# Kernel tuning notes

Hardware: AMD Instinct MI355X
Metric: run time of the kernel (lower is better)

The kernel has to match this reference:

```python
import jax, jax.numpy as jnp
import numpy as np

GRID_SIZE = 0.04   # matches init_kwargs grid_size
AXIS_CAP = 32      # max voxel bins per axis (1/0.04 = 25 < 32); keeps keys in int32 range


def setup_inputs() -> dict:
    key = jax.random.key(0)
    k1, k2 = jax.random.split(key)
    N, C = 1_000_000, 64
    coord = jax.random.uniform(k1, (N, 3), dtype=jnp.float32)   # points in unit cube
    feat = jax.random.normal(k2, (N, C), dtype=jnp.float32)
    # cumulative per-batch point counts (pointops offset convention), 4 equal batches
    offset = jnp.array([N // 4, N // 2, 3 * N // 4, N], dtype=jnp.int32)
    return {"coord": coord, "feat": feat, "offset": offset}


def reference(coord, feat, offset):
    N = coord.shape[0]
    B = offset.shape[0]
    # batch id per point from cumulative offsets
    batch = jnp.searchsorted(offset, jnp.arange(N, dtype=offset.dtype), side='right')  # [N]
    batch = batch.astype(jnp.int32)
    # voxelize_helper: start = per-batch min coord (start=None path)
    start = jax.ops.segment_min(coord, batch, num_segments=B)            # [B,3]
    vox = jnp.floor((coord - start[batch]) / GRID_SIZE).astype(jnp.int32)  # [N,3]
    # fused (batch, voxel) key; batches never share keys
    vkey = ((batch * AXIS_CAP + vox[:, 0]) * AXIS_CAP + vox[:, 1]) * AXIS_CAP + vox[:, 2]
    # sorted cluster indices + CSR-style segment ids
    order = jnp.argsort(vkey)                                            # sorted_cluster_indices
    skey = vkey[order]
    new_seg = jnp.concatenate([jnp.zeros((1,), jnp.int32),
                               (skey[1:] != skey[:-1]).astype(jnp.int32)])
    seg = jnp.cumsum(new_seg)                                            # [N] segment id per sorted point
    n_vox = seg[-1] + 1                                                  # actual number of voxels (traced)
    # segment_csr(coord[order], reduce='mean')
    counts = jax.ops.segment_sum(jnp.ones((N,), coord.dtype), seg, num_segments=N)  # [N] padded
    coord_out = jax.ops.segment_sum(coord[order], seg, num_segments=N) / jnp.maximum(counts, 1.0)[:, None]
    # segment_csr(feat[order], reduce='max')
    feat_out = jax.ops.segment_max(feat[order], seg, num_segments=N)
    valid = jnp.arange(N) < n_vox                                        # [N] pad mask
    coord_out = jnp.where(valid[:, None], coord_out, 0.0)
    feat_out = jnp.where(valid[:, None], feat_out, 0.0)
    # batch[idx_ptr[:-1]] -> batch of first point in each segment, then batch2offset
    batch_out = jax.ops.segment_min(batch[order], seg, num_segments=N)
    batch_out = jnp.where(valid, batch_out, B)                           # padded rows -> bucket B
    per_batch = jax.ops.segment_sum(jnp.ones((N,), jnp.int32), batch_out, num_segments=B + 1)[:B]
    offset_out = jnp.cumsum(per_batch)                                   # [B]
    # outputs padded to N rows; first n_vox rows are the real voxels
    return coord_out, feat_out, offset_out, n_vox
```

## Files before the change

### kernel.cpp

```cpp
#include <hip/hip_runtime.h>
#include <hip/hip_bf16.h>
#include <cstdint>

#define AXIS_CAP 32
#define GRID_SIZE_F 0.04f
#define BINS_PER_BATCH (AXIS_CAP * AXIS_CAP * AXIS_CAP)
#define SCAN_TPB 256
#define BINS_PER_THREAD 4
#define BINS_PER_BLOCK (SCAN_TPB * BINS_PER_THREAD)
#define KC_PPT 4

typedef float f32x4 __attribute__((ext_vector_type(4)));
typedef uint32_t u32x2 __attribute__((ext_vector_type(2)));

__device__ __forceinline__ int point_batch(int i, const int* offs, int B) {
    int b = 0;
    for (int k = 0; k < B; ++k) b += (offs[k] <= i);
    return b;
}

__global__ void init_kernel(uint32_t* binCount, int nbins, int* startBits, int B) {
    int i = blockIdx.x * blockDim.x + threadIdx.x;
    int stride = gridDim.x * blockDim.x;
    for (int v = i; v < nbins; v += stride) binCount[v] = 0;
    if (i < 3 * B) startBits[i] = 0x7F800000;
}

__global__ __launch_bounds__(256) void batch_min4_kernel(
        const float* __restrict__ coord, const int* __restrict__ offs,
        int B, int N, int* __restrict__ startBits) {
    __shared__ int smin[12];
    if (threadIdx.x < 12) smin[threadIdx.x] = 0x7F800000;
    __syncthreads();

    int o0 = offs[0];
    int o1 = (B > 1) ? offs[1] : o0;
    int o2 = (B > 2) ? offs[2] : o1;

    float m[4][3];
#pragma unroll
    for (int bb = 0; bb < 4; ++bb)
#pragma unroll
        for (int d = 0; d < 3; ++d) m[bb][d] = INFINITY;

    int gid = blockIdx.x * blockDim.x + threadIdx.x;
    int stride = gridDim.x * blockDim.x;
    for (int i = gid; i < N; i += stride) {
        float x = coord[(size_t)i * 3 + 0];
        float y = coord[(size_t)i * 3 + 1];
        float z = coord[(size_t)i * 3 + 2];
        int b = (i >= o0) + (i >= o1) + (i >= o2);
#pragma unroll
        for (int bb = 0; bb < 4; ++bb) {
            bool sel = (bb == b);
            m[bb][0] = fminf(m[bb][0], sel ? x : INFINITY);
            m[bb][1] = fminf(m[bb][1], sel ? y : INFINITY);
            m[bb][2] = fminf(m[bb][2], sel ? z : INFINITY);
        }
    }

#pragma unroll
    for (int bb = 0; bb < 4; ++bb)
#pragma unroll
        for (int d = 0; d < 3; ++d) {
            float v = m[bb][d];
            for (int off = 32; off > 0; off >>= 1)
                v = fminf(v, __shfl_xor(v, off));
            m[bb][d] = v;
        }

    if ((threadIdx.x & 63) == 0) {
#pragma unroll
        for (int bb = 0; bb < 4; ++bb)
#pragma unroll
            for (int d = 0; d < 3; ++d)
                atomicMin(&smin[bb * 3 + d], __float_as_int(m[bb][d]));
    }
    __syncthreads();
    if (threadIdx.x < 12 && (threadIdx.x / 3) < B)
        atomicMin(&startBits[threadIdx.x], smin[threadIdx.x]);
}

__global__ void batch_min_generic_kernel(const float* __restrict__ coord,
                                         const int* __restrict__ offs,
                                         int B, int N, int* startBits) {
    int i = blockIdx.x * blockDim.x + threadIdx.x;
    if (i >= N) return;
    int b = point_batch(i, offs, B);
    for (int d = 0; d < 3; ++d) {
        float c = coord[(size_t)i * 3 + d];
        atomicMin(&startBits[b * 3 + d], __float_as_int(c));
    }
}

__global__ __launch_bounds__(256) void keys_count4_kernel(
        const float* __restrict__ coord, const int* __restrict__ offs,
        const int* __restrict__ startBits, int B, int N,
        u32x2* __restrict__ kr, uint32_t* __restrict__ binCount) {
    int o0 = offs[0];
    int o1 = (B > 1) ? offs[1] : o0;
    int o2 = (B > 2) ? offs[2] : o1;
    float s00 = __int_as_float(startBits[0]);
    float s01 = __int_as_float(startBits[1]);
    float s02 = __int_as_float(startBits[2]);
    float s10 = (B > 1) ? __int_as_float(startBits[3]) : 0.f;
    float s11 = (B > 1) ? __int_as_float(startBits[4]) : 0.f;
    float s12 = (B > 1) ? __int_as_float(startBits[5]) : 0.f;
    float s20 = (B > 2) ? __int_as_float(startBits[6]) : 0.f;
    float s21 = (B > 2) ? __int_as_float(startBits[7]) : 0.f;
    float s22 = (B > 2) ? __int_as_float(startBits[8]) : 0.f;
    float s30 = (B > 3) ? __int_as_float(startBits[9]) : 0.f;
    float s31 = (B > 3) ? __int_as_float(startBits[10]) : 0.f;
    float s32 = (B > 3) ? __int_as_float(startBits[11]) : 0.f;

    int i0 = blockIdx.x * (256 * KC_PPT) + threadIdx.x;
#pragma unroll
    for (int j = 0; j < KC_PPT; ++j) {
        int i = i0 + j * 256;
        if (i >= N) continue;
        float x = coord[(size_t)i * 3 + 0];
        float y = coord[(size_t)i * 3 + 1];
        float z = coord[(size_t)i * 3 + 2];
        int b = (i >= o0) + (i >= o1) + (i >= o2);
        float sx = (b == 0) ? s00 : (b == 1) ? s10 : (b == 2) ? s20 : s30;
        float sy = (b == 0) ? s01 : (b == 1) ? s11 : (b == 2) ? s21 : s31;
        float sz = (b == 0) ? s02 : (b == 1) ? s12 : (b == 2) ? s22 : s32;
        int vx = (int)floorf((x - sx) / GRID_SIZE_F);
        int vy = (int)floorf((y - sy) / GRID_SIZE_F);
        int vz = (int)floorf((z - sz) / GRID_SIZE_F);
        vx = vx < 0 ? 0 : (vx > AXIS_CAP - 1 ? AXIS_CAP - 1 : vx);
        vy = vy < 0 ? 0 : (vy > AXIS_CAP - 1 ? AXIS_CAP - 1 : vy);
        vz = vz < 0 ? 0 : (vz > AXIS_CAP - 1 ? AXIS_CAP - 1 : vz);
        uint32_t key = ((uint32_t)b * AXIS_CAP + vx) * AXIS_CAP * AXIS_CAP
                     + (uint32_t)vy * AXIS_CAP + vz;
        uint32_t r = atomicAdd(&binCount[key], 1u);
        u32x2 kv = {key, r};
        kr[i] = kv;
    }
}

__global__ void keys_count_generic_kernel(
        const float* __restrict__ coord, const int* __restrict__ offs,
        const int* __restrict__ startBits, int B, int N,
        u32x2* __restrict__ kr, uint32_t* __restrict__ binCount) {
    int i = blockIdx.x * blockDim.x + threadIdx.x;
    if (i >= N) return;
    int b = point_batch(i, offs, B);
    int v[3];
    for (int d = 0; d < 3; ++d) {
        float s = __int_as_float(startBits[b * 3 + d]);
        float q = (coord[(size_t)i * 3 + d] - s) / GRID_SIZE_F;
        int vi = (int)floorf(q);
        vi = vi < 0 ? 0 : (vi > AXIS_CAP - 1 ? AXIS_CAP - 1 : vi);
        v[d] = vi;
    }
    uint32_t key = ((uint32_t)b * AXIS_CAP + v[0]) * AXIS_CAP * AXIS_CAP
                 + (uint32_t)v[1] * AXIS_CAP + v[2];
    uint32_t r = atomicAdd(&binCount[key], 1u);
    u32x2 kv = {key, r};
    kr[i] = kv;
}

__global__ void scan1_kernel(const uint32_t* __restrict__ binCount,
                             uint32_t* __restrict__ binStart,
                             uint32_t* __restrict__ binSeg,
                             uint32_t* __restrict__ blockCnt,
                             uint32_t* __restrict__ blockOcc) {
    __shared__ uint32_t sC[SCAN_TPB], sO[SCAN_TPB];
    int t = threadIdx.x;
    int base = blockIdx.x * BINS_PER_BLOCK + t * BINS_PER_THREAD;
    uint32_t c[BINS_PER_THREAD];
    uint32_t tc = 0, to = 0;
#pragma unroll
    for (int j = 0; j < BINS_PER_THREAD; ++j) {
        c[j] = binCount[base + j];
        tc += c[j];
        to += (c[j] > 0u);
    }
    sC[t] = tc; sO[t] = to;
    __syncthreads();
    for (int off = 1; off < SCAN_TPB; off <<= 1) {
        uint32_t a = 0, b2 = 0;
        if (t >= off) { a = sC[t - off]; b2 = sO[t - off]; }
        __syncthreads();
        sC[t] += a; sO[t] += b2;
        __syncthreads();
    }
    uint32_t exC = sC[t] - tc;
    uint32_t exO = sO[t] - to;
#pragma unroll
    for (int j = 0; j < BINS_PER_THREAD; ++j) {
        binStart[base + j] = exC;
        binSeg[base + j] = exO;
        exC += c[j];
        exO += (c[j] > 0u);
    }
    if (t == SCAN_TPB - 1) {
        blockCnt[blockIdx.x] = sC[t];
        blockOcc[blockIdx.x] = sO[t];
    }
}

__global__ void scan2_kernel(uint32_t* blockCnt, uint32_t* blockOcc,
                             uint32_t* totals, int nb) {
    __shared__ uint32_t sC[SCAN_TPB], sO[SCAN_TPB];
    int t = threadIdx.x;
    uint32_t c = (t < nb) ? blockCnt[t] : 0u;
    uint32_t o = (t < nb) ? blockOcc[t] : 0u;
    sC[t] = c; sO[t] = o;
    __syncthreads();
    for (int off = 1; off < SCAN_TPB; off <<= 1) {
        uint32_t a = 0, b2 = 0;
        if (t >= off) { a = sC[t - off]; b2 = sO[t - off]; }
        __syncthreads();
        sC[t] += a; sO[t] += b2;
        __syncthreads();
    }
    if (t < nb) { blockCnt[t] = sC[t] - c; blockOcc[t] = sO[t] - o; }
    if (t == SCAN_TPB - 1) { totals[0] = sO[t]; totals[1] = sC[t]; }
}

__global__ void scan3_kernel(uint32_t* __restrict__ binStart,
                             uint32_t* __restrict__ binSeg,
                             const uint32_t* __restrict__ blockCnt,
                             const uint32_t* __restrict__ blockOcc) {
    int t = threadIdx.x;
    int base = blockIdx.x * BINS_PER_BLOCK + t * BINS_PER_THREAD;
    uint32_t oc = blockCnt[blockIdx.x];
    uint32_t oo = blockOcc[blockIdx.x];
#pragma unroll
    for (int j = 0; j < BINS_PER_THREAD; ++j) {
        binStart[base + j] += oc;
        binSeg[base + j] += oo;
    }
}

__global__ void scatter_kernel(const u32x2* __restrict__ kr,
                               const uint32_t* __restrict__ binStart,
                               uint32_t* __restrict__ pointIdx, int N,
                               const uint32_t* __restrict__ binSeg,
                               const uint32_t* __restrict__ totals,
                               float* __restrict__ out, int B, int C) {
    int i = blockIdx.x * blockDim.x + threadIdx.x;
    if (blockIdx.x == 0 && threadIdx.x <= (unsigned)B) {
        uint32_t nvox = totals[0];
        float* tail = out + (size_t)N * 3 + (size_t)N * C;
        if (threadIdx.x < (unsigned)B) {
            uint32_t v = (threadIdx.x == (unsigned)(B - 1))
                             ? nvox
                             : binSeg[(size_t)(threadIdx.x + 1) * BINS_PER_BATCH];
            tail[threadIdx.x] = (float)v;
        }
        if (threadIdx.x == 0) tail[B] = (float)nvox;
    }
    if (i >= N) return;
    u32x2 k = __builtin_nontemporal_load(&kr[i]);
    pointIdx[binStart[k.x] + k.y] = (uint32_t)i;
}

__global__ __launch_bounds__(256) void reduce_kernel(
        const float* __restrict__ coord, const float* __restrict__ feat,
        const uint32_t* __restrict__ binCount,
        const uint32_t* __restrict__ binStart,
        const uint32_t* __restrict__ binSeg,
        const uint32_t* __restrict__ pointIdx,
        float* __restrict__ out, int N, int C) {
    int wid = (blockIdx.x << 2) + (threadIdx.x >> 6);
    int lane = threadIdx.x & 63;
    uint32_t cnt = binCount[wid];
    if (cnt == 0u) return;
    float* feat_out = out + (size_t)N * 3;

    uint32_t st = binStart[wid];
    uint32_t seg = binSeg[wid];
    float sx = 0.f, sy = 0.f, sz = 0.f;

    if (C == 64) {
        float m = -INFINITY;
        for (uint32_t base = 0; base < cnt; base += 64) {
            uint32_t nchunk = min(64u, cnt - base);
            bool valid = lane < (int)nchunk;
            uint32_t myIdx =
                valid ? __builtin_nontemporal_load(&pointIdx[st + base + lane])
                      : 0u;
            if (valid) {
                const float* cp = coord + (size_t)myIdx * 3;
                sx += cp[0]; sy += cp[1]; sz += cp[2];
            }
            for (uint32_t p = 0; p < nchunk; p += 16) {
                float v[16];
#pragma unroll
                for (int j = 0; j < 16; ++j) {
                    uint32_t pp = min(p + (uint32_t)j, nchunk - 1u);
                    uint32_t idx = __shfl(myIdx, (int)pp);
                    v[j] = __builtin_nontemporal_load(
                        &feat[(size_t)idx * 64 + lane]);
                }
#pragma unroll
                for (int s = 1; s < 16; s <<= 1)
#pragma unroll
                    for (int j = 0; j < 16; j += 2 * s)
                        v[j] = fmaxf(v[j], v[j + s]);
                m = fmaxf(m, v[0]);
            }
        }
        __builtin_nontemporal_store(m, &feat_out[(size_t)seg * 64 + lane]);
    } else {
        for (uint32_t p = lane; p < cnt; p += 64) {
            uint32_t idx = pointIdx[st + p];
            sx += coord[(size_t)idx * 3 + 0];
            sy += coord[(size_t)idx * 3 + 1];
            sz += coord[(size_t)idx * 3 + 2];
        }
        for (int c = lane; c < C; c += 64) {
            float m = -INFINITY;
            for (uint32_t p = 0; p < cnt; ++p) {
                uint32_t idx = pointIdx[st + p];
                m = fmaxf(m, feat[(size_t)idx * C + c]);
            }
            feat_out[(size_t)seg * C + c] = m;
        }
    }

    for (int off = 32; off > 0; off >>= 1) {
        sx += __shfl_xor(sx, off);
        sy += __shfl_xor(sy, off);
        sz += __shfl_xor(sz, off);
    }
    if (lane == 0) {
        float inv = 1.0f / (float)cnt;
        out[(size_t)seg * 3 + 0] = sx * inv;
        out[(size_t)seg * 3 + 1] = sy * inv;
        out[(size_t)seg * 3 + 2] = sz * inv;
    }
}

__global__ __launch_bounds__(256) void pad_kernel(
        float* __restrict__ out, const uint32_t* __restrict__ totals,
        int N, int C) {
    uint32_t nvox = totals[0];
    uint32_t tid = (uint32_t)blockIdx.x * blockDim.x + threadIdx.x;
    uint32_t nthreads = (uint32_t)gridDim.x * blockDim.x;
    uint32_t rows = (uint32_t)N - nvox;
    float* featBase = out + (size_t)N * 3;
    if ((C & 3) == 0) {
        f32x4 z4 = {0.f, 0.f, 0.f, 0.f};
        uint32_t quadsTotal = rows * (uint32_t)(C >> 2);
        f32x4* padBase = (f32x4*)(featBase + (size_t)nvox * C);
        for (uint32_t q = tid; q < quadsTotal; q += nthreads)
            __builtin_nontemporal_store(z4, &padBase[q]);
    } else {
        uint32_t eTotal = rows * (uint32_t)C;
        float* padBase = featBase + (size_t)nvox * C;
        for (uint32_t e = tid; e < eTotal; e += nthreads)
            __builtin_nontemporal_store(0.f, &padBase[e]);
    }
    {
        uint32_t cTotal = rows * 3u;
        float* cBase = out + (size_t)nvox * 3;
        for (uint32_t e = tid; e < cTotal; e += nthreads)
            __builtin_nontemporal_store(0.f, &cBase[e]);
    }
}

extern "C" void kernel_launch(void* const* d_in, const int* in_sizes, int n_in,
                              void* d_out, int out_size, void* d_ws, size_t ws_size,
                              hipStream_t stream) {
    const float* coord = (const float*)d_in[0];
    const float* feat  = (const float*)d_in[1];
    const int*   offs  = (const int*)d_in[2];
    float* out = (float*)d_out;

    int N = in_sizes[0] / 3;
    int C = in_sizes[1] / N;
    int B = in_sizes[2];
    int NBINS = B * BINS_PER_BATCH;
    int NB1 = NBINS / BINS_PER_BLOCK;

    uint8_t* w = (uint8_t*)d_ws;
    uint32_t* binCount = (uint32_t*)w;              w += (size_t)NBINS * 4;
    uint32_t* binStart = (uint32_t*)w;              w += (size_t)NBINS * 4;
    uint32_t* binSeg   = (uint32_t*)w;              w += (size_t)NBINS * 4;
    uint32_t* blockCnt = (uint32_t*)w;              w += (size_t)NB1 * 4;
    uint32_t* blockOcc = (uint32_t*)w;              w += (size_t)NB1 * 4;
    uint32_t* totals   = (uint32_t*)w;              w += 2 * 4;
    int*      startBits= (int*)w;                   w += (size_t)3 * B * 4 + 8;
    u32x2*    kr       = (u32x2*)w;                 w += (size_t)N * 8;
    uint32_t* pointIdx = (uint32_t*)w;

    int ptBlocks = (N + 255) / 256;
    int kcBlocks = (N + 256 * KC_PPT - 1) / (256 * KC_PPT);

    init_kernel<<<512, 256, 0, stream>>>(binCount, NBINS, startBits, B);
    if (B <= 4) {
        batch_min4_kernel<<<1024, 256, 0, stream>>>(coord, offs, B, N, startBits);
        keys_count4_kernel<<<kcBlocks, 256, 0, stream>>>(coord, offs, startBits,
                                                         B, N, kr, binCount);
    } else {
        batch_min_generic_kernel<<<ptBlocks, 256, 0, stream>>>(coord, offs, B, N,
                                                               startBits);
        keys_count_generic_kernel<<<ptBlocks, 256, 0, stream>>>(coord, offs,
                                                                startBits, B, N,
                                                                kr, binCount);
    }
    scan1_kernel<<<NB1, SCAN_TPB, 0, stream>>>(binCount, binStart, binSeg,
                                               blockCnt, blockOcc);
    scan2_kernel<<<1, SCAN_TPB, 0, stream>>>(blockCnt, blockOcc, totals, NB1);
    scan3_kernel<<<NB1, SCAN_TPB, 0, stream>>>(binStart, binSeg, blockCnt, blockOcc);
    scatter_kernel<<<ptBlocks, 256, 0, stream>>>(kr, binStart, pointIdx, N,
                                                 binSeg, totals, out, B, C);
    reduce_kernel<<<NBINS / 4, 256, 0, stream>>>(coord, feat, binCount, binStart,
                                                 binSeg, pointIdx, out, N, C);
    pad_kernel<<<2048, 256, 0, stream>>>(out, totals, N, C);
}
```

Measured before the change: 230.6 us.

## Compact occupied bins into a list and fuse padding into reduce kernel

The scan stage now writes a compacted list of occupied bin ids indexed by segment, so each reduce wavefront handles a real voxel (wave id equals segment id) rather than idling on empty bins. The separate pad kernel is folded into the reduce kernel, whose grid-stride loop zero-fills the padded rows, removing one launch. Nontemporal loads on pointIdx and feat are replaced by ordinary loads. The reduce grid still covers all bins, so many waves now only do padding work, and the extra occList array adds workspace traffic.

```diff
diff --git a/kernel.cpp b/kernel.cpp
--- a/kernel.cpp
+++ b/kernel.cpp
@@ -220,8 +220,10 @@
     if (t == SCAN_TPB - 1) { totals[0] = sO[t]; totals[1] = sC[t]; }
 }
 
-__global__ void scan3_kernel(uint32_t* __restrict__ binStart,
+__global__ void scan3_kernel(const uint32_t* __restrict__ binCount,
+                             uint32_t* __restrict__ binStart,
                              uint32_t* __restrict__ binSeg,
+                             uint32_t* __restrict__ occList,
                              const uint32_t* __restrict__ blockCnt,
                              const uint32_t* __restrict__ blockOcc) {
     int t = threadIdx.x;
@@ -230,8 +232,10 @@
     uint32_t oo = blockOcc[blockIdx.x];
 #pragma unroll
     for (int j = 0; j < BINS_PER_THREAD; ++j) {
+        uint32_t seg = binSeg[base + j] + oo;
         binStart[base + j] += oc;
-        binSeg[base + j] += oo;
+        binSeg[base + j] = seg;
+        if (binCount[base + j] > 0u) occList[seg] = (uint32_t)(base + j);
     }
 }
 
@@ -262,96 +266,91 @@
         const float* __restrict__ coord, const float* __restrict__ feat,
         const uint32_t* __restrict__ binCount,
         const uint32_t* __restrict__ binStart,
-        const uint32_t* __restrict__ binSeg,
+        const uint32_t* __restrict__ occList,
         const uint32_t* __restrict__ pointIdx,
+        const uint32_t* __restrict__ totals,
         float* __restrict__ out, int N, int C) {
     int wid = (blockIdx.x << 2) + (threadIdx.x >> 6);
     int lane = threadIdx.x & 63;
-    uint32_t cnt = binCount[wid];
-    if (cnt == 0u) return;
+    uint32_t nvox = totals[0];
     float* feat_out = out + (size_t)N * 3;
 
-    uint32_t st = binStart[wid];
-    uint32_t seg = binSeg[wid];
-    float sx = 0.f, sy = 0.f, sz = 0.f;
-
-    if (C == 64) {
-        float m = -INFINITY;
-        for (uint32_t base = 0; base < cnt; base += 64) {
-            uint32_t nchunk = min(64u, cnt - base);
-            bool valid = lane < (int)nchunk;
-            uint32_t myIdx =
-                valid ? __builtin_nontemporal_load(&pointIdx[st + base + lane])
-                      : 0u;
-            if (valid) {
-                const float* cp = coord + (size_t)myIdx * 3;
-                sx += cp[0]; sy += cp[1]; sz += cp[2];
+    if ((uint32_t)wid < nvox) {
+        int bin = (int)occList[wid];
+        uint32_t cnt = binCount[bin];
+        uint32_t st = binStart[bin];
+        uint32_t seg = (uint32_t)wid;
+        float sx = 0.f, sy = 0.f, sz = 0.f;
+
+        if (C == 64) {
+            float m = -INFINITY;
+            for (uint32_t base = 0; base < cnt; base += 64) {
+                uint32_t nchunk = min(64u, cnt - base);
+                bool valid = lane < (int)nchunk;
+                uint32_t myIdx = valid ? pointIdx[st + base + lane] : 0u;
+                if (valid) {
+                    const float* cp = coord + (size_t)myIdx * 3;
+                    sx += cp[0]; sy += cp[1]; sz += cp[2];
+                }
+                for (uint32_t p = 0; p < nchunk; p += 16) {
+                    float v[16];
+#pragma unroll
+                    for (int j = 0; j < 16; ++j) {
+                        uint32_t pp = min(p + (uint32_t)j, nchunk - 1u);
+                        uint32_t idx = __shfl(myIdx, (int)pp);
+                        v[j] = feat[(size_t)idx * 64 + lane];
+                    }
+#pragma unroll
+                    for (int s = 1; s < 16; s <<= 1)
+#pragma unroll
+                        for (int j = 0; j < 16; j += 2 * s)
+                            v[j] = fmaxf(v[j], v[j + s]);
+                    m = fmaxf(m, v[0]);
+                }
             }
-            for (uint32_t p = 0; p < nchunk; p += 16) {
-                float v[16];
-#pragma unroll
-                for (int j = 0; j < 16; ++j) {
-                    uint32_t pp = min(p + (uint32_t)j, nchunk - 1u);
-                    uint32_t idx = __shfl(myIdx, (int)pp);
-                    v[j] = __builtin_nontemporal_load(
-                        &feat[(size_t)idx * 64 + lane]);
+            __builtin_nontemporal_store(m, &feat_out[(size_t)seg * 64 + lane]);
+        } else {
+            for (uint32_t p = lane; p < cnt; p += 64) {
+                uint32_t idx = pointIdx[st + p];
+                sx += coord[(size_t)idx * 3 + 0];
+                sy += coord[(size_t)idx * 3 + 1];
+                sz += coord[(size_t)idx * 3 + 2];
+            }
+            for (int c = lane; c < C; c += 64) {
+                float m = -INFINITY;
+                for (uint32_t p = 0; p < cnt; ++p) {
+                    uint32_t idx = pointIdx[st + p];
+                    m = fmaxf(m, feat[(size_t)idx * C + c]);
                 }
-#pragma unroll
-                for (int s = 1; s < 16; s <<= 1)
-#pragma unroll
-                    for (int j = 0; j < 16; j += 2 * s)
-                        v[j] = fmaxf(v[j], v[j + s]);
-                m = fmaxf(m, v[0]);
+                feat_out[(size_t)seg * C + c] = m;
             }
         }
-        __builtin_nontemporal_store(m, &feat_out[(size_t)seg * 64 + lane]);
-    } else {
-        for (uint32_t p = lane; p < cnt; p += 64) {
-            uint32_t idx = pointIdx[st + p];
-            sx += coord[(size_t)idx * 3 + 0];
-            sy += coord[(size_t)idx * 3 + 1];
-            sz += coord[(size_t)idx * 3 + 2];
-        }
-        for (int c = lane; c < C; c += 64) {
-            float m = -INFINITY;
-            for (uint32_t p = 0; p < cnt; ++p) {
-                uint32_t idx = pointIdx[st + p];
-                m = fmaxf(m, feat[(size_t)idx * C + c]);
-            }
-            feat_out[(size_t)seg * C + c] = m;
-        }
-    }
-
-    for (int off = 32; off > 0; off >>= 1) {
-        sx += __shfl_xor(sx, off);
-        sy += __shfl_xor(sy, off);
-        sz += __shfl_xor(sz, off);
-    }
-    if (lane == 0) {
-        float inv = 1.0f / (float)cnt;
-        out[(size_t)seg * 3 + 0] = sx * inv;
-        out[(size_t)seg * 3 + 1] = sy * inv;
-        out[(size_t)seg * 3 + 2] = sz * inv;
-    }
-}
-
-__global__ __launch_bounds__(256) void pad_kernel(
-        float* __restrict__ out, const uint32_t* __restrict__ totals,
-        int N, int C) {
-    uint32_t nvox = totals[0];
+
+        for (int off = 32; off > 0; off >>= 1) {
+            sx += __shfl_xor(sx, off);
+            sy += __shfl_xor(sy, off);
+            sz += __shfl_xor(sz, off);
+        }
+        if (lane == 0) {
+            float inv = 1.0f / (float)cnt;
+            out[(size_t)seg * 3 + 0] = sx * inv;
+            out[(size_t)seg * 3 + 1] = sy * inv;
+            out[(size_t)seg * 3 + 2] = sz * inv;
+        }
+    }
+
     uint32_t tid = (uint32_t)blockIdx.x * blockDim.x + threadIdx.x;
     uint32_t nthreads = (uint32_t)gridDim.x * blockDim.x;
     uint32_t rows = (uint32_t)N - nvox;
-    float* featBase = out + (size_t)N * 3;
     if ((C & 3) == 0) {
         f32x4 z4 = {0.f, 0.f, 0.f, 0.f};
         uint32_t quadsTotal = rows * (uint32_t)(C >> 2);
-        f32x4* padBase = (f32x4*)(featBase + (size_t)nvox * C);
+        f32x4* padBase = (f32x4*)(feat_out + (size_t)nvox * C);
         for (uint32_t q = tid; q < quadsTotal; q += nthreads)
             __builtin_nontemporal_store(z4, &padBase[q]);
     } else {
         uint32_t eTotal = rows * (uint32_t)C;
-        float* padBase = featBase + (size_t)nvox * C;
+        float* padBase = feat_out + (size_t)nvox * C;
         for (uint32_t e = tid; e < eTotal; e += nthreads)
             __builtin_nontemporal_store(0.f, &padBase[e]);
     }
@@ -381,6 +380,7 @@
     uint32_t* binCount = (uint32_t*)w;              w += (size_t)NBINS * 4;
     uint32_t* binStart = (uint32_t*)w;              w += (size_t)NBINS * 4;
     uint32_t* binSeg   = (uint32_t*)w;              w += (size_t)NBINS * 4;
+    uint32_t* occList  = (uint32_t*)w;              w += (size_t)NBINS * 4;
     uint32_t* blockCnt = (uint32_t*)w;              w += (size_t)NB1 * 4;
     uint32_t* blockOcc = (uint32_t*)w;              w += (size_t)NB1 * 4;
     uint32_t* totals   = (uint32_t*)w;              w += 2 * 4;
@@ -406,10 +406,11 @@
     scan1_kernel<<<NB1, SCAN_TPB, 0, stream>>>(binCount, binStart, binSeg,
                                                blockCnt, blockOcc);
     scan2_kernel<<<1, SCAN_TPB, 0, stream>>>(blockCnt, blockOcc, totals, NB1);
-    scan3_kernel<<<NB1, SCAN_TPB, 0, stream>>>(binStart, binSeg, blockCnt, blockOcc);
+    scan3_kernel<<<NB1, SCAN_TPB, 0, stream>>>(binCount, binStart, binSeg,
+                                               occList, blockCnt, blockOcc);
     scatter_kernel<<<ptBlocks, 256, 0, stream>>>(kr, binStart, pointIdx, N,
                                                  binSeg, totals, out, B, C);
     reduce_kernel<<<NBINS / 4, 256, 0, stream>>>(coord, feat, binCount, binStart,
-                                                 binSeg, pointIdx, out, N, C);
-    pad_kernel<<<2048, 256, 0, stream>>>(out, totals, N, C);
-}
+                                                 occList, pointIdx, totals, out,
+                                                 N, C);
+}
```

Result: faster. 188.8 us (median of 2 runs) (-18.1%).
